# Kernel optimization log

Measured on AMD Instinct MI355X. Metric: run time of the kernel, lower is better.

Reference implementation:

```python
import jax, jax.numpy as jnp
import numpy as np

DIM = 512
CODEBOOK_SIZE = 8192
B, N = 8, 2048
EPS = 1e-12


def setup_inputs() -> dict:
    key = jax.random.key(0)
    k1, k2, k3 = jax.random.split(key, 3)
    x = jax.random.normal(k1, (B, N, DIM), dtype=jnp.float32)
    # matches torch.randn(codebook_size, dim) * dim ** -0.5
    codebook = jax.random.normal(k2, (CODEBOOK_SIZE, DIM), dtype=jnp.float32) * DIM ** -0.5
    # nn.Linear(dim, dim, bias=False) weight, applied as x @ W.T
    W = jax.random.normal(k3, (DIM, DIM), dtype=jnp.float32) * DIM ** -0.5
    return {"x": x, "codebook": codebook, "W": W}


def _l2norm(t):
    return t / jnp.maximum(jnp.linalg.norm(t, axis=-1, keepdims=True), EPS)


def _rotate_from_to(q, x):
    """Rotation trick: forward value == q, gradient flows through x via a
    detached Householder-style rotation (R = I - 2ww^T + 2 q_hat x_hat^T)
    and detached norm rescaling."""
    sg = jax.lax.stop_gradient
    norm_x = jnp.linalg.norm(x, axis=-1, keepdims=True)
    norm_q = jnp.linalg.norm(q, axis=-1, keepdims=True)
    x_hat = x / jnp.maximum(norm_x, EPS)
    q_hat = q / jnp.maximum(norm_q, EPS)
    w = sg(_l2norm(x_hat + q_hat))
    x_hat_d, q_hat_d = sg(x_hat), sg(q_hat)
    e = x
    rotated = (e
               - 2.0 * jnp.sum(e * w, axis=-1, keepdims=True) * w
               + 2.0 * jnp.sum(e * x_hat_d, axis=-1, keepdims=True) * q_hat_d)
    return rotated * sg(norm_q / jnp.maximum(norm_x, EPS))


def reference(x, codebook, W):
    # implicit codebook = Linear(codebook)
    codes = jnp.einsum('cd,ed->ce', codebook, W)  # [C, d]
    d2 = -2.0 * jnp.einsum('bnd,cd->bnc', x, codes) + jnp.sum(codes * codes, axis=-1)
    indices = jnp.argmin(jax.lax.stop_gradient(d2), axis=-1)  # [b, n] int
    quantized = codes[indices]  # gather -> [b, n, d]
    commit_loss = jnp.mean((jax.lax.stop_gradient(x) - quantized) ** 2)
    quantized = _rotate_from_to(quantized, x)
    return quantized, indices, commit_loss
```

## Files before the change

kernel.cpp:

```cpp
#include <hip/hip_runtime.h>


#define DIMK  512
#define CBN   8192
#define MROWS 16384

#define SX 24.0f
#define SC 500.0f
#define INV_SS (1.0f / (SX * SC))
#define DKEY  1231
#define NSLOT 3

#define WS_CODES   0UL
#define WS_XQ      16777216UL
#define WS_CQ      25165824UL
#define WS_NORMS   29360128UL
#define WS_CAND    29392896UL
#define WS_CBH     29392896UL
#define WS_CBL     37781504UL
#define WS_WH      54558720UL
#define WS_WL      55083008UL
#define WS_LOSSP   55607296UL

typedef short s16x8 __attribute__((ext_vector_type(8)));
typedef int   i32x4 __attribute__((ext_vector_type(4)));
typedef float f32x4 __attribute__((ext_vector_type(4)));

__device__ __forceinline__ unsigned short f2bf(float f) {
    unsigned u = __float_as_uint(f);
    unsigned r = u + 0x7FFFu + ((u >> 16) & 1u);
    return (unsigned short)(r >> 16);
}
__device__ __forceinline__ float bf2f(unsigned short h) {
    return __uint_as_float(((unsigned)h) << 16);
}
__device__ __forceinline__ void load_lds16(const void* g, void* l) {
    __builtin_amdgcn_global_load_lds((const __attribute__((address_space(1))) void*)g,
                                     (__attribute__((address_space(3))) void*)l,
                                     16, 0, 0);
}
__device__ __forceinline__ signed char q8(float v, float s) {
    return (signed char)__float2int_rn(fminf(fmaxf(v * s, -127.0f), 127.0f));
}

__global__ __launch_bounds__(256) void prep(
        const float* __restrict__ x, const float* __restrict__ cb, const float* __restrict__ W,
        signed char* __restrict__ xq,
        unsigned short* __restrict__ cbh, unsigned short* __restrict__ cbl,
        unsigned short* __restrict__ wh, unsigned short* __restrict__ wl,
        float* __restrict__ norms) {
    const int b = blockIdx.x;
    const int t = threadIdx.x;
    if (b < 8192) {
        const int i = b * 256 + t;
        float4 v = ((const float4*)x)[i];
        char4 c;
        c.x = q8(v.x, SX); c.y = q8(v.y, SX); c.z = q8(v.z, SX); c.w = q8(v.w, SX);
        ((char4*)xq)[i] = c;
    } else if (b < 12288) {
        const int i = (b - 8192) * 256 + t;
        float4 v = ((const float4*)cb)[i];
        ushort4 h, l;
        h.x = f2bf(v.x); l.x = f2bf(v.x - bf2f(h.x));
        h.y = f2bf(v.y); l.y = f2bf(v.y - bf2f(h.y));
        h.z = f2bf(v.z); l.z = f2bf(v.z - bf2f(h.z));
        h.w = f2bf(v.w); l.w = f2bf(v.w - bf2f(h.w));
        ((ushort4*)cbh)[i] = h;
        ((ushort4*)cbl)[i] = l;
    } else if (b < 12544) {
        const int i = (b - 12288) * 256 + t;
        float4 v = ((const float4*)W)[i];
        ushort4 h, l;
        h.x = f2bf(v.x); l.x = f2bf(v.x - bf2f(h.x));
        h.y = f2bf(v.y); l.y = f2bf(v.y - bf2f(h.y));
        h.z = f2bf(v.z); l.z = f2bf(v.z - bf2f(h.z));
        h.w = f2bf(v.w); l.w = f2bf(v.w - bf2f(h.w));
        ((ushort4*)wh)[i] = h;
        ((ushort4*)wl)[i] = l;
    } else {
        const int i = (b - 12544) * 256 + t;
        norms[i] = 0.0f;
    }
}

__global__ __launch_bounds__(256) void codes_mfma(
        const unsigned short* __restrict__ Ah_g, const unsigned short* __restrict__ Al_g,
        const unsigned short* __restrict__ Bh_g, const unsigned short* __restrict__ Bl_g,
        float* __restrict__ C, signed char* __restrict__ Cq, float* __restrict__ Norms) {
    __shared__ __align__(16) unsigned short Ahi[128 * 32];
    __shared__ __align__(16) unsigned short Alo[128 * 32];
    __shared__ __align__(16) unsigned short Bhi[128 * 32];
    __shared__ __align__(16) unsigned short Blo[128 * 32];

    const int t    = threadIdx.x;
    const int w    = t >> 6;
    const int lane = t & 63;
    const int quad = lane >> 4;
    const int l16  = lane & 15;
    const int wm   = w & 1, wn = w >> 1;
    const int rowBase = blockIdx.x * 128;
    const int colBase = blockIdx.y * 128;

    f32x4 acc[4][4];
    #pragma unroll
    for (int i = 0; i < 4; ++i)
        #pragma unroll
        for (int j = 0; j < 4; ++j)
            acc[i][j] = (f32x4)(0.0f);

    const int mr = t >> 2;
    const int kq = ((t & 3) ^ ((t >> 3) & 3)) * 8;
    const size_t gxa = (size_t)(rowBase + mr) * DIMK + kq;
    const size_t gxb = gxa + (size_t)64 * DIMK;
    const size_t gca = (size_t)(colBase + mr) * DIMK + kq;
    const size_t gcb = gca + (size_t)64 * DIMK;
    const int l0 = w * 512;
    const int l1 = 2048 + w * 512;

    const int swz8 = (quad ^ ((l16 >> 1) & 3)) * 8;

    for (int k0 = 0; k0 < DIMK; k0 += 32) {
        load_lds16(Ah_g + gxa + k0, &Ahi[l0]);
        load_lds16(Ah_g + gxb + k0, &Ahi[l1]);
        load_lds16(Al_g + gxa + k0, &Alo[l0]);
        load_lds16(Al_g + gxb + k0, &Alo[l1]);
        load_lds16(Bh_g + gca + k0, &Bhi[l0]);
        load_lds16(Bh_g + gcb + k0, &Bhi[l1]);
        load_lds16(Bl_g + gca + k0, &Blo[l0]);
        load_lds16(Bl_g + gcb + k0, &Blo[l1]);
        __syncthreads();

        s16x8 ah[4], al[4], bh[4], bl[4];
        #pragma unroll
        for (int i = 0; i < 4; ++i) {
            const int m = wm * 64 + i * 16 + l16;
            ah[i] = *(const s16x8*)&Ahi[m * 32 + swz8];
            al[i] = *(const s16x8*)&Alo[m * 32 + swz8];
        }
        #pragma unroll
        for (int j = 0; j < 4; ++j) {
            const int n = wn * 64 + j * 16 + l16;
            bh[j] = *(const s16x8*)&Bhi[n * 32 + swz8];
            bl[j] = *(const s16x8*)&Blo[n * 32 + swz8];
        }
        #pragma unroll
        for (int i = 0; i < 4; ++i)
            #pragma unroll
            for (int j = 0; j < 4; ++j) {
                acc[i][j] = __builtin_amdgcn_mfma_f32_16x16x32_bf16(ah[i], bh[j], acc[i][j], 0, 0, 0);
                acc[i][j] = __builtin_amdgcn_mfma_f32_16x16x32_bf16(ah[i], bl[j], acc[i][j], 0, 0, 0);
                acc[i][j] = __builtin_amdgcn_mfma_f32_16x16x32_bf16(al[i], bh[j], acc[i][j], 0, 0, 0);
            }
        __syncthreads();
    }

    #pragma unroll
    for (int i = 0; i < 4; ++i) {
        #pragma unroll
        for (int r = 0; r < 4; ++r) {
            const int row = rowBase + wm * 64 + i * 16 + quad * 4 + r;
            float nsum = 0.0f;
            #pragma unroll
            for (int j = 0; j < 4; ++j) {
                const int col = colBase + wn * 64 + j * 16 + l16;
                const float v = acc[i][j][r];
                C[(size_t)row * DIMK + col] = v;
                Cq[(size_t)row * DIMK + col] = q8(v, SC);
                nsum = fmaf(v, v, nsum);
            }
            nsum += __shfl_xor(nsum, 1, 64);
            nsum += __shfl_xor(nsum, 2, 64);
            nsum += __shfl_xor(nsum, 4, 64);
            nsum += __shfl_xor(nsum, 8, 64);
            if (l16 == 0) atomicAdd(&Norms[row], nsum);
        }
    }
}

__global__ __launch_bounds__(512, 6) void d2_argmin_i8(
        const signed char* __restrict__ Xq,
        const signed char* __restrict__ Cq,
        const float* __restrict__ Norms,
        unsigned* __restrict__ Cand) {
    __shared__ __align__(16) signed char Ash[128 * 64];
    __shared__ __align__(16) signed char Bsh[128 * 64];

    const int t    = threadIdx.x;
    const int w    = t >> 6;
    const int lane = t & 63;
    const int quad = lane >> 4;
    const int l16  = lane & 15;
    const int wm   = w & 3, wn = w >> 2;
    const int rowBase = blockIdx.x * 128;
    const int colBase = blockIdx.y * 128;

    i32x4 acc[2][4];
    #pragma unroll
    for (int i = 0; i < 2; ++i)
        #pragma unroll
        for (int j = 0; j < 4; ++j)
            acc[i][j] = (i32x4)(0);

    const int mr  = t >> 2;
    const int kcs = ((t & 3) ^ ((t >> 3) & 3)) * 16;
    const size_t gxa = (size_t)(rowBase + mr) * DIMK + kcs;
    const size_t gca = (size_t)(colBase + mr) * DIMK + kcs;
    const int lb = w * 1024;

    const int swz  = (quad ^ ((l16 >> 1) & 3)) * 16;
    const int aoff = (wm * 32 + l16) * 64 + swz;
    const int boff = (wn * 64 + l16) * 64 + swz;

    float nq[4];
    #pragma unroll
    for (int j = 0; j < 4; ++j)
        nq[j] = fmaf(Norms[colBase + wn * 64 + j * 16 + l16], 4096.0f, 65536.0f);

    for (int k0 = 0; k0 < DIMK; k0 += 64) {
        load_lds16(Xq + gxa + k0, &Ash[lb]);
        load_lds16(Cq + gca + k0, &Bsh[lb]);
        __syncthreads();

        i32x4 af[2];
        af[0] = *(const i32x4*)&Ash[aoff];
        af[1] = *(const i32x4*)&Ash[aoff + 1024];
        #pragma unroll
        for (int j = 0; j < 4; ++j) {
            const i32x4 bfj = *(const i32x4*)&Bsh[boff + j * 1024];
            acc[0][j] = __builtin_amdgcn_mfma_i32_16x16x64_i8(af[0], bfj, acc[0][j], 0, 0, 0);
            acc[1][j] = __builtin_amdgcn_mfma_i32_16x16x64_i8(af[1], bfj, acc[1][j], 0, 0, 0);
        }
        __syncthreads();
    }

    const unsigned colG = colBase + wn * 64 + l16;
    const int subtile = blockIdx.y * 2 + wn;
    const float C2 = -8192.0f * INV_SS;

    #pragma unroll
    for (int i = 0; i < 2; ++i) {
        #pragma unroll
        for (int r = 0; r < 4; ++r) {
            unsigned k[4];
            #pragma unroll
            for (int j = 0; j < 4; ++j) {
                const float kf = fmaf((float)acc[i][j][r], C2, nq[j]);
                int ki = (int)kf;
                ki = ki < 0 ? 0 : ki;
                ki = ki > 524287 ? 524287 : ki;
                k[j] = ((unsigned)ki << 13) | (colG + j * 16);
            }
            unsigned lo01 = min(k[0], k[1]), hi01 = max(k[0], k[1]);
            unsigned lo23 = min(k[2], k[3]), hi23 = max(k[2], k[3]);
            unsigned a0 = min(lo01, lo23);
            unsigned m  = max(lo01, lo23);
            unsigned tt = min(hi01, hi23);
            unsigned a1 = min(m, tt);
            unsigned a2 = max(m, tt);
            #pragma unroll
            for (int mk = 1; mk < 16; mk <<= 1) {
                const unsigned b0 = __shfl_xor(a0, mk, 64);
                const unsigned b1 = __shfl_xor(a1, mk, 64);
                const unsigned b2 = __shfl_xor(a2, mk, 64);
                const unsigned M0 = max(a0, b0);
                const unsigned m1 = min(a1, b1);
                const unsigned n0 = min(a0, b0);
                a2 = min(max(m1, M0), min(a2, b2));
                a1 = min(M0, m1);
                a0 = n0;
            }
            if (l16 == 0) {
                const int row = rowBase + wm * 32 + i * 16 + quad * 4 + r;
                unsigned* slot = Cand + ((size_t)row * 128 + subtile) * NSLOT;
                slot[0] = a0; slot[1] = a1; slot[2] = a2;
            }
        }
    }
}

__global__ __launch_bounds__(256) void refine_gather(
        const float* __restrict__ X, const float* __restrict__ Codes,
        const float* __restrict__ Norms, const unsigned* __restrict__ Cand,
        float* __restrict__ outQ, float* __restrict__ outIdx,
        float* __restrict__ lossP) {
    const int t    = threadIdx.x;
    const int w    = t >> 6;
    const int lane = t & 63;
    const int row  = blockIdx.x * 4 + w;

    const unsigned* cp = Cand + (size_t)row * 128 * NSLOT + lane * 6;
    unsigned sl[6];
    #pragma unroll
    for (int s = 0; s < 6; ++s) sl[s] = cp[s];

    unsigned mn = sl[0];
    #pragma unroll
    for (int s = 1; s < 6; ++s) mn = min(mn, sl[s]);
    #pragma unroll
    for (int mask = 1; mask < 64; mask <<= 1)
        mn = min(mn, (unsigned)__shfl((int)mn, lane ^ mask, 64));
    const unsigned thrp = (((mn >> 13) + DKEY) << 13) | 0x1FFFu;

    const float4 xa = *(const float4*)(X + (size_t)row * DIMK + lane * 8);
    const float4 xb = *(const float4*)(X + (size_t)row * DIMK + lane * 8 + 4);

    float bestD = __builtin_inff();
    unsigned bestIdx = 0xFFFFFFFFu;

    #pragma unroll
    for (int s = 0; s < 6; ++s) {
        unsigned long long bm = __ballot(sl[s] <= thrp);
        while (bm) {
            const int src = __ffsll(bm) - 1;
            bm &= bm - 1;
            const unsigned sv = (unsigned)__shfl((int)sl[s], src, 64);
            const unsigned idx = sv & 0x1FFFu;
            const float4 ca = *(const float4*)(Codes + (size_t)idx * DIMK + lane * 8);
            const float4 cbv = *(const float4*)(Codes + (size_t)idx * DIMK + lane * 8 + 4);
            float s2 = xa.x * ca.x + xa.y * ca.y + xa.z * ca.z + xa.w * ca.w
                     + xb.x * cbv.x + xb.y * cbv.y + xb.z * cbv.z + xb.w * cbv.w;
            #pragma unroll
            for (int mm = 1; mm < 64; mm <<= 1) s2 += __shfl_xor(s2, mm, 64);
            const float d2 = fmaf(-2.0f, s2, Norms[idx]);
            if (d2 < bestD || (d2 == bestD && idx < bestIdx)) { bestD = d2; bestIdx = idx; }
        }
    }

    const float4 qa = *(const float4*)(Codes + (size_t)bestIdx * DIMK + lane * 8);
    const float4 qb = *(const float4*)(Codes + (size_t)bestIdx * DIMK + lane * 8 + 4);
    *(float4*)(outQ + (size_t)row * DIMK + lane * 8) = qa;
    *(float4*)(outQ + (size_t)row * DIMK + lane * 8 + 4) = qb;
    float dx0 = xa.x - qa.x, dx1 = xa.y - qa.y, dx2 = xa.z - qa.z, dx3 = xa.w - qa.w;
    float dy0 = xb.x - qb.x, dy1 = xb.y - qb.y, dy2 = xb.z - qb.z, dy3 = xb.w - qb.w;
    float s = dx0 * dx0 + dx1 * dx1 + dx2 * dx2 + dx3 * dx3
            + dy0 * dy0 + dy1 * dy1 + dy2 * dy2 + dy3 * dy3;
    #pragma unroll
    for (int off = 32; off > 0; off >>= 1) s += __shfl_down(s, off);
    if (lane == 0) {
        lossP[row] = s;
        outIdx[row] = (float)bestIdx;
    }
}

__global__ __launch_bounds__(256) void finalize_loss(const float* __restrict__ lossPartials,
                                                     float* __restrict__ outLoss) {
    const int t = threadIdx.x;
    float s = 0.0f;
    for (int i = t; i < MROWS; i += 256) s += lossPartials[i];
    #pragma unroll
    for (int off = 32; off > 0; off >>= 1) s += __shfl_down(s, off);
    __shared__ float red[4];
    if ((t & 63) == 0) red[t >> 6] = s;
    __syncthreads();
    if (t == 0)
        *outLoss = (red[0] + red[1] + red[2] + red[3]) * (1.0f / (float)((size_t)MROWS * DIMK));
}

extern "C" void kernel_launch(void* const* d_in, const int* in_sizes, int n_in,
                              void* d_out, int out_size, void* d_ws, size_t ws_size,
                              hipStream_t stream) {
    const float* x  = (const float*)d_in[0];
    const float* cb = (const float*)d_in[1];
    const float* W  = (const float*)d_in[2];
    float* out = (float*)d_out;

    char* ws = (char*)d_ws;
    float* codes          = (float*)(ws + WS_CODES);
    signed char* xq       = (signed char*)(ws + WS_XQ);
    signed char* cq       = (signed char*)(ws + WS_CQ);
    float* norms          = (float*)(ws + WS_NORMS);
    unsigned* cand        = (unsigned*)(ws + WS_CAND);
    unsigned short* cbh   = (unsigned short*)(ws + WS_CBH);
    unsigned short* cbl   = (unsigned short*)(ws + WS_CBL);
    unsigned short* wh    = (unsigned short*)(ws + WS_WH);
    unsigned short* wl    = (unsigned short*)(ws + WS_WL);
    float* lossP          = (float*)(ws + WS_LOSSP);

    prep<<<12576, 256, 0, stream>>>(x, cb, W, xq, cbh, cbl, wh, wl, norms);

    codes_mfma<<<dim3(CBN / 128, DIMK / 128), 256, 0, stream>>>(cbh, cbl, wh, wl, codes, cq, norms);

    d2_argmin_i8<<<dim3(MROWS / 128, CBN / 128), 512, 0, stream>>>(xq, cq, norms, cand);

    refine_gather<<<MROWS / 4, 256, 0, stream>>>(x, codes, norms, cand, out,
                                                 out + (size_t)MROWS * DIMK, lossP);
    finalize_loss<<<1, 256, 0, stream>>>(lossP, out + (size_t)MROWS * DIMK + MROWS);
}
```

Baseline: 292.5 us.

## Double-buffer LDS tiles in codes GEMM and int8 distance kernel

Both the bf16-split codes GEMM and the int8 distance/argmin kernel now use two LDS buffers, so the next K-slice is loaded while MFMAs run on the current one. This replaces the load-sync-compute-sync loop with one barrier per step and an explicit vmcnt wait. LDS per block doubles, which can lower occupancy, especially for the 512-thread d2 kernel that requests 6 blocks per CU.

```diff
diff --git a/kernel.cpp b/kernel.cpp
--- a/kernel.cpp
+++ b/kernel.cpp
@@ -87,10 +87,10 @@
         const unsigned short* __restrict__ Ah_g, const unsigned short* __restrict__ Al_g,
         const unsigned short* __restrict__ Bh_g, const unsigned short* __restrict__ Bl_g,
         float* __restrict__ C, signed char* __restrict__ Cq, float* __restrict__ Norms) {
-    __shared__ __align__(16) unsigned short Ahi[128 * 32];
-    __shared__ __align__(16) unsigned short Alo[128 * 32];
-    __shared__ __align__(16) unsigned short Bhi[128 * 32];
-    __shared__ __align__(16) unsigned short Blo[128 * 32];
+    __shared__ __align__(16) unsigned short Ahi[2][128 * 32];
+    __shared__ __align__(16) unsigned short Alo[2][128 * 32];
+    __shared__ __align__(16) unsigned short Bhi[2][128 * 32];
+    __shared__ __align__(16) unsigned short Blo[2][128 * 32];
 
     const int t    = threadIdx.x;
     const int w    = t >> 6;
@@ -119,40 +119,63 @@
 
     const int swz8 = (quad ^ ((l16 >> 1) & 3)) * 8;
 
-    for (int k0 = 0; k0 < DIMK; k0 += 32) {
-        load_lds16(Ah_g + gxa + k0, &Ahi[l0]);
-        load_lds16(Ah_g + gxb + k0, &Ahi[l1]);
-        load_lds16(Al_g + gxa + k0, &Alo[l0]);
-        load_lds16(Al_g + gxb + k0, &Alo[l1]);
-        load_lds16(Bh_g + gca + k0, &Bhi[l0]);
-        load_lds16(Bh_g + gcb + k0, &Bhi[l1]);
-        load_lds16(Bl_g + gca + k0, &Blo[l0]);
-        load_lds16(Bl_g + gcb + k0, &Blo[l1]);
+#define CODES_STAGE(NXT, K0)                                   \
+    do {                                                       \
+        load_lds16(Ah_g + gxa + (K0), &Ahi[NXT][l0]);          \
+        load_lds16(Ah_g + gxb + (K0), &Ahi[NXT][l1]);          \
+        load_lds16(Al_g + gxa + (K0), &Alo[NXT][l0]);          \
+        load_lds16(Al_g + gxb + (K0), &Alo[NXT][l1]);          \
+        load_lds16(Bh_g + gca + (K0), &Bhi[NXT][l0]);          \
+        load_lds16(Bh_g + gcb + (K0), &Bhi[NXT][l1]);          \
+        load_lds16(Bl_g + gca + (K0), &Blo[NXT][l0]);          \
+        load_lds16(Bl_g + gcb + (K0), &Blo[NXT][l1]);          \
+    } while (0)
+
+#define CODES_COMPUTE(CUR)                                                                         \
+    do {                                                                                           \
+        s16x8 ah[4], al[4], bh[4], bl[4];                                                          \
+        _Pragma("unroll")                                                                          \
+        for (int i = 0; i < 4; ++i) {                                                              \
+            const int m = wm * 64 + i * 16 + l16;                                                  \
+            ah[i] = *(const s16x8*)&Ahi[CUR][m * 32 + swz8];                                       \
+            al[i] = *(const s16x8*)&Alo[CUR][m * 32 + swz8];                                       \
+        }                                                                                          \
+        _Pragma("unroll")                                                                          \
+        for (int j = 0; j < 4; ++j) {                                                              \
+            const int n = wn * 64 + j * 16 + l16;                                                  \
+            bh[j] = *(const s16x8*)&Bhi[CUR][n * 32 + swz8];                                       \
+            bl[j] = *(const s16x8*)&Blo[CUR][n * 32 + swz8];                                       \
+        }                                                                                          \
+        _Pragma("unroll")                                                                          \
+        for (int i = 0; i < 4; ++i)                                                                \
+            _Pragma("unroll")                                                                      \
+            for (int j = 0; j < 4; ++j) {                                                          \
+                acc[i][j] = __builtin_amdgcn_mfma_f32_16x16x32_bf16(ah[i], bh[j], acc[i][j], 0, 0, 0); \
+                acc[i][j] = __builtin_amdgcn_mfma_f32_16x16x32_bf16(ah[i], bl[j], acc[i][j], 0, 0, 0); \
+                acc[i][j] = __builtin_amdgcn_mfma_f32_16x16x32_bf16(al[i], bh[j], acc[i][j], 0, 0, 0); \
+            }                                                                                      \
+    } while (0)
+
+    CODES_STAGE(0, 0);
+    asm volatile("s_waitcnt vmcnt(0)" ::: "memory");
+    __syncthreads();
+
+    for (int k0 = 0; k0 < DIMK; k0 += 64) {
+        CODES_STAGE(1, k0 + 32);
+        CODES_COMPUTE(0);
+        asm volatile("s_waitcnt vmcnt(0)" ::: "memory");
         __syncthreads();
-
-        s16x8 ah[4], al[4], bh[4], bl[4];
-        #pragma unroll
-        for (int i = 0; i < 4; ++i) {
-            const int m = wm * 64 + i * 16 + l16;
-            ah[i] = *(const s16x8*)&Ahi[m * 32 + swz8];
-            al[i] = *(const s16x8*)&Alo[m * 32 + swz8];
+        if (k0 + 64 < DIMK) {
+            CODES_STAGE(0, k0 + 64);
+            CODES_COMPUTE(1);
+            asm volatile("s_waitcnt vmcnt(0)" ::: "memory");
+            __syncthreads();
+        } else {
+            CODES_COMPUTE(1);
         }
-        #pragma unroll
-        for (int j = 0; j < 4; ++j) {
-            const int n = wn * 64 + j * 16 + l16;
-            bh[j] = *(const s16x8*)&Bhi[n * 32 + swz8];
-            bl[j] = *(const s16x8*)&Blo[n * 32 + swz8];
-        }
-        #pragma unroll
-        for (int i = 0; i < 4; ++i)
-            #pragma unroll
-            for (int j = 0; j < 4; ++j) {
-                acc[i][j] = __builtin_amdgcn_mfma_f32_16x16x32_bf16(ah[i], bh[j], acc[i][j], 0, 0, 0);
-                acc[i][j] = __builtin_amdgcn_mfma_f32_16x16x32_bf16(ah[i], bl[j], acc[i][j], 0, 0, 0);
-                acc[i][j] = __builtin_amdgcn_mfma_f32_16x16x32_bf16(al[i], bh[j], acc[i][j], 0, 0, 0);
-            }
-        __syncthreads();
-    }
+    }
+#undef CODES_STAGE
+#undef CODES_COMPUTE
 
     #pragma unroll
     for (int i = 0; i < 4; ++i) {
@@ -182,8 +205,8 @@
         const signed char* __restrict__ Cq,
         const float* __restrict__ Norms,
         unsigned* __restrict__ Cand) {
-    __shared__ __align__(16) signed char Ash[128 * 64];
-    __shared__ __align__(16) signed char Bsh[128 * 64];
+    __shared__ __align__(16) signed char Ash[2][128 * 64];
+    __shared__ __align__(16) signed char Bsh[2][128 * 64];
 
     const int t    = threadIdx.x;
     const int w    = t >> 6;
@@ -216,22 +239,40 @@
     for (int j = 0; j < 4; ++j)
         nq[j] = fmaf(Norms[colBase + wn * 64 + j * 16 + l16], 4096.0f, 65536.0f);
 
-    for (int k0 = 0; k0 < DIMK; k0 += 64) {
-        load_lds16(Xq + gxa + k0, &Ash[lb]);
-        load_lds16(Cq + gca + k0, &Bsh[lb]);
-        __syncthreads();
-
-        i32x4 af[2];
-        af[0] = *(const i32x4*)&Ash[aoff];
-        af[1] = *(const i32x4*)&Ash[aoff + 1024];
-        #pragma unroll
-        for (int j = 0; j < 4; ++j) {
-            const i32x4 bfj = *(const i32x4*)&Bsh[boff + j * 1024];
-            acc[0][j] = __builtin_amdgcn_mfma_i32_16x16x64_i8(af[0], bfj, acc[0][j], 0, 0, 0);
-            acc[1][j] = __builtin_amdgcn_mfma_i32_16x16x64_i8(af[1], bfj, acc[1][j], 0, 0, 0);
-        }
-        __syncthreads();
-    }
+#define D2_STEP(CUR, NXT, K0, DO_STAGE, DO_SYNC)                                                   \
+    do {                                                                                           \
+        if (DO_STAGE) {                                                                            \
+            load_lds16(Xq + gxa + (K0) + 64, &Ash[NXT][lb]);                                       \
+            load_lds16(Cq + gca + (K0) + 64, &Bsh[NXT][lb]);                                       \
+        }                                                                                          \
+        i32x4 af0 = *(const i32x4*)&Ash[CUR][aoff];                                                \
+        i32x4 af1 = *(const i32x4*)&Ash[CUR][aoff + 1024];                                         \
+        _Pragma("unroll")                                                                          \
+        for (int j = 0; j < 4; ++j) {                                                              \
+            const i32x4 bfj = *(const i32x4*)&Bsh[CUR][boff + j * 1024];                           \
+            acc[0][j] = __builtin_amdgcn_mfma_i32_16x16x64_i8(af0, bfj, acc[0][j], 0, 0, 0);       \
+            acc[1][j] = __builtin_amdgcn_mfma_i32_16x16x64_i8(af1, bfj, acc[1][j], 0, 0, 0);       \
+        }                                                                                          \
+        if (DO_SYNC) {                                                                             \
+            asm volatile("s_waitcnt vmcnt(0)" ::: "memory");                                       \
+            __syncthreads();                                                                       \
+        }                                                                                          \
+    } while (0)
+
+    load_lds16(Xq + gxa, &Ash[0][lb]);
+    load_lds16(Cq + gca, &Bsh[0][lb]);
+    asm volatile("s_waitcnt vmcnt(0)" ::: "memory");
+    __syncthreads();
+
+    D2_STEP(0, 1,   0, true,  true);
+    D2_STEP(1, 0,  64, true,  true);
+    D2_STEP(0, 1, 128, true,  true);
+    D2_STEP(1, 0, 192, true,  true);
+    D2_STEP(0, 1, 256, true,  true);
+    D2_STEP(1, 0, 320, true,  true);
+    D2_STEP(0, 1, 384, true,  true);
+    D2_STEP(1, 0, 448, false, false);
+#undef D2_STEP
 
     const unsigned colG = colBase + wn * 64 + l16;
     const int subtile = blockIdx.y * 2 + wn;
```

Result: no change. 292.7 us (+0.1%).
